# Performance work log

Measured on AMD Instinct MI355X. Metric: run time of the kernel, lower is better.

The kernel has to match this reference:

```python
import jax, jax.numpy as jnp
import numpy as np
from jax import lax

B, T, D, H, L = 16, 256, 128, 128, 4  # batch, seq, input_size, hidden, num_layers
NUM_CLASSES = 10
EPS = 1e-5


def instancenorm(x):
    # x: [B, T, C]; InstanceNorm1d normalizes over the length dim (T) per (B, C),
    # biased variance, eps=1e-5, no affine.
    m = x.mean(axis=1, keepdims=True)
    v = x.var(axis=1, keepdims=True)
    return (x - m) / jnp.sqrt(v + EPS)


def lstm_stack(x, Wih, Whh, bih, bhh):
    # x: [B, T, I]; Wih/Whh: [L, 4H, I_or_H]; bih/bhh: [L, 4H]. Gate order i,f,g,o.
    batch = x.shape[0]
    hid = Whh.shape[-1]
    out = x
    for l in range(Wih.shape[0]):
        wih, whh, b = Wih[l], Whh[l], bih[l] + bhh[l]
        h0 = jnp.zeros((batch, hid), dtype=x.dtype)
        c0 = jnp.zeros((batch, hid), dtype=x.dtype)
        xs = out.swapaxes(0, 1)  # [T, B, I]

        def step(carry, xt):
            h, c = carry
            g = xt @ wih.T + h @ whh.T + b
            i, f, gg, o = jnp.split(g, 4, axis=-1)
            c_new = jax.nn.sigmoid(f) * c + jax.nn.sigmoid(i) * jnp.tanh(gg)
            h_new = jax.nn.sigmoid(o) * jnp.tanh(c_new)
            return (h_new, c_new), h_new

        _, hs = lax.scan(step, (h0, c0), xs)
        out = hs.swapaxes(0, 1)  # [B, T, H]
    return out


def setup_inputs() -> dict:
    key = jax.random.key(0)
    ks = jax.random.split(key, 16)
    s = 1.0 / np.sqrt(H)
    u = lambda k, shape: jax.random.uniform(k, shape, jnp.float32, -s, s)
    return {
        "x": jax.random.normal(ks[0], (B, T, D), jnp.float32),
        "Wih": u(ks[1], (L, 4 * H, D)),   # input_size == hidden_size so shapes stack
        "Whh": u(ks[2], (L, 4 * H, H)),
        "bih": u(ks[3], (L, 4 * H)),
        "bhh": u(ks[4], (L, 4 * H)),
        "proj_h_w": u(ks[5], (H, H)),
        "proj_h_b": u(ks[6], (H,)),
        "proj_x_w": u(ks[7], (H, D)),
        "proj_x_b": u(ks[8], (H,)),
        "attn_w": u(ks[9], (H,)),
        "fc_w": u(ks[10], (NUM_CLASSES, H)),
        "fc_b": u(ks[11], (NUM_CLASSES,)),
    }


def reference(x, Wih, Whh, bih, bhh, proj_h_w, proj_h_b, proj_x_w, proj_x_b, attn_w, fc_w, fc_b):
    batch, seq_len, input_dim = x.shape
    # normalize(): means/stdev are detached; torch std is unbiased (ddof=1)
    means = lax.stop_gradient(x.mean(axis=(0, 1), keepdims=True))
    stdev = lax.stop_gradient(x.std(axis=(0, 1), ddof=1, keepdims=True) + EPS)
    x = (x - means) / stdev
    x = instancenorm(x)

    lstm_out = lstm_stack(x, Wih, Whh, bih, bhh)   # dropout is identity in eval
    lstm_out = instancenorm(lstm_out)

    ph = lstm_out @ proj_h_w.T + proj_h_b           # [B, T, H]
    px = x @ proj_x_w.T + proj_x_b                  # [B, T, H]
    px = instancenorm(px)

    # additive attention over expanded [B, T, D, H] (values identical across D,
    # matching the original broadcast/expand semantics)
    combined = jnp.tanh(
        jnp.broadcast_to((ph + px)[:, :, None, :], (batch, seq_len, input_dim, ph.shape[-1]))
    )
    logits = jnp.einsum("btdh,h->btd", combined, attn_w)       # [B, T, D]
    alpha = jax.nn.softmax(logits.reshape(batch, -1), axis=1)   # softmax over T*D
    attention_map = alpha.reshape(batch, seq_len, input_dim)

    # classify: context = sum over (T, D) of lstm_out_ex * alpha
    context = jnp.einsum("bth,btd->bh", ph, attention_map)      # [B, H]
    out = context @ fc_w.T + fc_b                               # [B, num_classes]
    return out, attention_map
```

## Files before the change

kernel.cpp:

```cpp
#include <hip/hip_runtime.h>
#include <math.h>
#include <cstddef>

#define B_ 16
#define T_ 256
#define D_ 128
#define H_ 128
#define L_ 4
#define G_ 512
#define NC_ 10
#define EPS_ 1e-5f
#define C_ 16
#define NCHUNK_ (T_ / C_)

#define HROW_ 144
#define HOFF(k) ((k) + (((k) >> 5) << 2))

typedef float f4v __attribute__((ext_vector_type(4)));

#define LOAD_W8(w, base)                                                   \
    asm volatile(                                                          \
        "global_load_dwordx4 %0, %8, off\n\t"                             \
        "global_load_dwordx4 %1, %8, off offset:16\n\t"                   \
        "global_load_dwordx4 %2, %8, off offset:32\n\t"                   \
        "global_load_dwordx4 %3, %8, off offset:48\n\t"                   \
        "global_load_dwordx4 %4, %8, off offset:64\n\t"                   \
        "global_load_dwordx4 %5, %8, off offset:80\n\t"                   \
        "global_load_dwordx4 %6, %8, off offset:96\n\t"                   \
        "global_load_dwordx4 %7, %8, off offset:112\n\t"                  \
        "s_waitcnt vmcnt(0)"                                               \
        : "=&v"(w[0]), "=&v"(w[1]), "=&v"(w[2]), "=&v"(w[3]),              \
          "=&v"(w[4]), "=&v"(w[5]), "=&v"(w[6]), "=&v"(w[7])               \
        : "v"(base)                                                        \
        : "memory")

#define DOT32R(dst_, warr_, hvarr_)                                        \
    {                                                                      \
        float d0_ = 0.f, d1_ = 0.f;                                        \
        _Pragma("unroll")                                                  \
        for (int j_ = 0; j_ < 8; j_++) {                                   \
            d0_ = fmaf(warr_[j_].x, hvarr_[j_].x, d0_);                    \
            d1_ = fmaf(warr_[j_].y, hvarr_[j_].y, d1_);                    \
            d0_ = fmaf(warr_[j_].z, hvarr_[j_].z, d0_);                    \
            d1_ = fmaf(warr_[j_].w, hvarr_[j_].w, d1_);                    \
        }                                                                  \
        dst_ = d0_ + d1_;                                                  \
    }

__device__ __forceinline__ float sigmoid_(float x) {
    x = fminf(fmaxf(x, -30.f), 30.f);
    return 1.f / (1.f + __expf(-x));
}
__device__ __forceinline__ float tanh_(float x) {
    float ax = fminf(fabsf(x), 15.f);
    float e = __expf(2.f * ax);
    float t = 1.f - 2.f / (e + 1.f);
    return copysignf(t, x);
}
__device__ __forceinline__ void wait_ge_(int* p, int v) {
    if (__hip_atomic_load(p, __ATOMIC_RELAXED, __HIP_MEMORY_SCOPE_AGENT) < v) {
        do { __builtin_amdgcn_s_sleep(1); }
        while (__hip_atomic_load(p, __ATOMIC_RELAXED, __HIP_MEMORY_SCOPE_AGENT) < v);
    }
    (void)__hip_atomic_load(p, __ATOMIC_ACQUIRE, __HIP_MEMORY_SCOPE_AGENT);
}

__global__ __launch_bounds__(512) void stats_bd(const float* __restrict__ x,
                                                float* __restrict__ sum_bd,
                                                float* __restrict__ sq_bd) {
    int b = blockIdx.x;
    int tid = threadIdx.x;
    int d = tid & 127, r = tid >> 7;
    const float* xb = x + (size_t)b * T_ * D_;
    float s = 0.f, q = 0.f;
    for (int t = r; t < T_; t += 4) {
        float v = xb[t * D_ + d];
        s += v; q += v * v;
    }
    __shared__ float ls[512], lq[512];
    ls[tid] = s; lq[tid] = q;
    __syncthreads();
    if (r == 0) {
        s = ls[d] + ls[d + 128] + ls[d + 256] + ls[d + 384];
        q = lq[d] + lq[d + 128] + lq[d + 256] + lq[d + 384];
        sum_bd[b * 128 + d] = s;
        sq_bd[b * 128 + d] = q;
    }
}

__global__ __launch_bounds__(128) void stats_d(const float* __restrict__ sum_bd,
                                               const float* __restrict__ sq_bd,
                                               float* __restrict__ sdv) {
    int d = threadIdx.x;
    float s = 0.f, q = 0.f;
    for (int b = 0; b < B_; b++) { s += sum_bd[b * 128 + d]; q += sq_bd[b * 128 + d]; }
    float n = (float)(B_ * T_);
    float m = s / n;
    float varu = (q - n * m * m) / (n - 1.f);
    varu = fmaxf(varu, 0.f);
    sdv[d] = sqrtf(varu) + EPS_;
}

__global__ __launch_bounds__(256) void normalize_x(const float* __restrict__ x,
                                                   const float* __restrict__ sum_bd,
                                                   const float* __restrict__ sq_bd,
                                                   const float* __restrict__ sdv,
                                                   float* __restrict__ xn) {
    int idx = blockIdx.x * 256 + threadIdx.x;
    int d = idx & 127;
    int b = idx >> 15;
    int bd = b * 128 + d;
    float mu = sum_bd[bd] * (1.f / T_);
    float varT = sq_bd[bd] * (1.f / T_) - mu * mu;
    float s = sdv[d];
    float inv = rsqrtf(fmaxf(varT, 0.f) + EPS_ * s * s);
    xn[idx] = (x[idx] - mu) * inv;
}

__global__ __launch_bounds__(256) void gemm_bias_k128(const float* __restrict__ A,
                                                      const float* __restrict__ Bw,
                                                      const float* __restrict__ b1,
                                                      const float* __restrict__ b2,
                                                      float* __restrict__ C, int N) {
    __shared__ __align__(16) float As[16][64];
    __shared__ __align__(16) float Bs[16][64];
    int tid = threadIdx.x;
    int m0 = blockIdx.x * 64, n0 = blockIdx.y * 64;
    int lr = tid >> 2;
    int lc = (tid & 3) << 2;
    int tm = (tid >> 4) << 2;
    int tn = (tid & 15) << 2;
    float acc[4][4] = {};
    const float* Arow = A + (size_t)(m0 + lr) * 128 + lc;
    const float* Brow = Bw + (size_t)(n0 + lr) * 128 + lc;
    for (int kb = 0; kb < 128; kb += 16) {
        float4 av = *(const float4*)(Arow + kb);
        float4 bv = *(const float4*)(Brow + kb);
        __syncthreads();
        As[lc + 0][lr] = av.x; As[lc + 1][lr] = av.y; As[lc + 2][lr] = av.z; As[lc + 3][lr] = av.w;
        Bs[lc + 0][lr] = bv.x; Bs[lc + 1][lr] = bv.y; Bs[lc + 2][lr] = bv.z; Bs[lc + 3][lr] = bv.w;
        __syncthreads();
#pragma unroll
        for (int k = 0; k < 16; k++) {
            float4 a4 = *(const float4*)&As[k][tm];
            float4 b4 = *(const float4*)&Bs[k][tn];
            float ar[4] = {a4.x, a4.y, a4.z, a4.w};
            float br[4] = {b4.x, b4.y, b4.z, b4.w};
#pragma unroll
            for (int i = 0; i < 4; i++)
#pragma unroll
                for (int j = 0; j < 4; j++)
                    acc[i][j] = fmaf(ar[i], br[j], acc[i][j]);
        }
    }
#pragma unroll
    for (int i = 0; i < 4; i++) {
        int row = m0 + tm + i;
#pragma unroll
        for (int j = 0; j < 4; j++) {
            int col = n0 + tn + j;
            float bias = b1[col] + (b2 ? b2[col] : 0.f);
            C[(size_t)row * N + col] = acc[i][j] + bias;
        }
    }
}

__global__ __launch_bounds__(256) void gemm_norm_k128(const float* __restrict__ A,
                                                      const float* __restrict__ mu,
                                                      const float* __restrict__ inv,
                                                      const float* __restrict__ Bw,
                                                      const float* __restrict__ b1,
                                                      float* __restrict__ C, int N) {
    __shared__ __align__(16) float As[16][64];
    __shared__ __align__(16) float Bs[16][64];
    int tid = threadIdx.x;
    int m0 = blockIdx.x * 64, n0 = blockIdx.y * 64;
    int lr = tid >> 2;
    int lc = (tid & 3) << 2;
    int tm = (tid >> 4) << 2;
    int tn = (tid & 15) << 2;
    float acc[4][4] = {};
    int bidx = (m0 + lr) >> 8;
    const float* Arow = A + (size_t)(m0 + lr) * 128 + lc;
    const float* Brow = Bw + (size_t)(n0 + lr) * 128 + lc;
    const float* mup = mu + bidx * 128 + lc;
    const float* ivp = inv + bidx * 128 + lc;
    for (int kb = 0; kb < 128; kb += 16) {
        float4 av = *(const float4*)(Arow + kb);
        float4 m4 = *(const float4*)(mup + kb);
        float4 i4 = *(const float4*)(ivp + kb);
        av.x = (av.x - m4.x) * i4.x; av.y = (av.y - m4.y) * i4.y;
        av.z = (av.z - m4.z) * i4.z; av.w = (av.w - m4.w) * i4.w;
        float4 bv = *(const float4*)(Brow + kb);
        __syncthreads();
        As[lc + 0][lr] = av.x; As[lc + 1][lr] = av.y; As[lc + 2][lr] = av.z; As[lc + 3][lr] = av.w;
        Bs[lc + 0][lr] = bv.x; Bs[lc + 1][lr] = bv.y; Bs[lc + 2][lr] = bv.z; Bs[lc + 3][lr] = bv.w;
        __syncthreads();
#pragma unroll
        for (int k = 0; k < 16; k++) {
            float4 a4 = *(const float4*)&As[k][tm];
            float4 b4 = *(const float4*)&Bs[k][tn];
            float ar[4] = {a4.x, a4.y, a4.z, a4.w};
            float br[4] = {b4.x, b4.y, b4.z, b4.w};
#pragma unroll
            for (int i = 0; i < 4; i++)
#pragma unroll
                for (int j = 0; j < 4; j++)
                    acc[i][j] = fmaf(ar[i], br[j], acc[i][j]);
        }
    }
#pragma unroll
    for (int i = 0; i < 4; i++) {
        int row = m0 + tm + i;
#pragma unroll
        for (int j = 0; j < 4; j++) {
            int col = n0 + tn + j;
            C[(size_t)row * N + col] = acc[i][j] + b1[col];
        }
    }
}

__global__ __attribute__((amdgpu_waves_per_eu(2, 2))) __launch_bounds__(512)
void scan_pipe4(const float* __restrict__ g0,
                const float* __restrict__ Wih, const float* __restrict__ Whh,
                const float* __restrict__ bih, const float* __restrict__ bhh,
                float* __restrict__ h_glob,
                float* __restrict__ ring,
                int* __restrict__ flag_h,
                int* __restrict__ flag_g) {
    const int wg = blockIdx.x;
    const int tid = threadIdx.x;
    const int r = tid >> 2, q = tid & 3;

    if (wg < 64) {
        const int l = wg >> 4, b = wg & 15;
        __shared__ __align__(16) float hsh[2][HROW_];
        f4v w0[8], w1[8], w2[8], w3[8];
        const float* wl = Whh + (size_t)l * G_ * 128;
        LOAD_W8(w0, wl + ((size_t)(0 * 128 + r)) * 128 + q * 32);
        LOAD_W8(w1, wl + ((size_t)(1 * 128 + r)) * 128 + q * 32);
        LOAD_W8(w2, wl + ((size_t)(2 * 128 + r)) * 128 + q * 32);
        LOAD_W8(w3, wl + ((size_t)(3 * 128 + r)) * 128 + q * 32);
        float c = 0.f;
        if (tid < HROW_) hsh[0][tid] = 0.f;
        const float* g0p = g0 + (size_t)b * T_ * G_;
        const float* rsl = (l > 0) ? ring + ((size_t)(l - 1) * 16 + b) * (4 * C_ * G_) : ring;
        float* hob = h_glob + ((size_t)l * 16 + b) * T_ * 128;
        int* fg = (l > 0) ? flag_g + (l - 1) * 16 + b : flag_g;
        int* fh = flag_h + l * 16 + b;
        float hreg[C_];
        __syncthreads();

        for (int k = 0; k < NCHUNK_; k++) {
            if (l > 0) {
                if (tid == 0) wait_ge_(fg, k + 1);
                __syncthreads();
            }
#pragma unroll
            for (int half = 0; half < 2; half++) {
                float p0[8], p1[8], p2[8], p3[8];
#pragma unroll
                for (int s8 = 0; s8 < 8; s8++) {
                    int s = half * 8 + s8;
                    if (l == 0) {
                        const float* gp = g0p + (size_t)(k * C_ + s) * G_;
                        p0[s8] = gp[r]; p1[s8] = gp[128 + r];
                        p2[s8] = gp[256 + r]; p3[s8] = gp[384 + r];
                    } else {
                        const float* gp = rsl + ((size_t)(k & 3) * C_ + s) * G_;
                        p0[s8] = __hip_atomic_load(gp + r, __ATOMIC_RELAXED, __HIP_MEMORY_SCOPE_AGENT);
                        p1[s8] = __hip_atomic_load(gp + 128 + r, __ATOMIC_RELAXED, __HIP_MEMORY_SCOPE_AGENT);
                        p2[s8] = __hip_atomic_load(gp + 256 + r, __ATOMIC_RELAXED, __HIP_MEMORY_SCOPE_AGENT);
                        p3[s8] = __hip_atomic_load(gp + 384 + r, __ATOMIC_RELAXED, __HIP_MEMORY_SCOPE_AGENT);
                    }
                }
#pragma unroll
                for (int s8 = 0; s8 < 8; s8++) {
                    int s = half * 8 + s8;
                    int t = k * C_ + s;
                    const f4v* hb4 = (const f4v*)(hsh[t & 1] + q * 36);
                    f4v hv[8];
#pragma unroll
                    for (int j = 0; j < 8; j++) hv[j] = hb4[j];
                    float zi, zf, zg, zo;
                    DOT32R(zi, w0, hv);
                    DOT32R(zf, w1, hv);
                    DOT32R(zg, w2, hv);
                    DOT32R(zo, w3, hv);
                    zi += __shfl_xor(zi, 1); zi += __shfl_xor(zi, 2);
                    zf += __shfl_xor(zf, 1); zf += __shfl_xor(zf, 2);
                    zg += __shfl_xor(zg, 1); zg += __shfl_xor(zg, 2);
                    zo += __shfl_xor(zo, 1); zo += __shfl_xor(zo, 2);
                    zi += p0[s8]; zf += p1[s8]; zg += p2[s8]; zo += p3[s8];
                    float ai = sigmoid_(zi), af = sigmoid_(zf);
                    float ag = tanh_(zg),    ao = sigmoid_(zo);
                    c = fmaf(af, c, ai * ag);
                    float hn = ao * tanh_(c);
                    if (q == 0) hsh[(t + 1) & 1][HOFF(r)] = hn;
                    hreg[s] = hn;
                    __syncthreads();
                }
            }
            if (q == 0) {
#pragma unroll
                for (int s = 0; s < C_; s++)
                    __hip_atomic_store(hob + (size_t)(k * C_ + s) * 128 + r, hreg[s],
                                       __ATOMIC_RELAXED, __HIP_MEMORY_SCOPE_AGENT);
            }
            __syncthreads();
            if (tid == 0) __hip_atomic_store(fh, k + 1, __ATOMIC_RELEASE, __HIP_MEMORY_SCOPE_AGENT);
        }
    } else {
        const int li = (wg - 64) >> 4;
        const int l = li + 1, b = (wg - 64) & 15;
        __shared__ __align__(16) float hch[C_][HROW_];
        f4v w0[8], w1[8], w2[8], w3[8];
        const float* wl = Wih + (size_t)l * G_ * 128;
        LOAD_W8(w0, wl + ((size_t)(0 * 128 + r)) * 128 + q * 32);
        LOAD_W8(w1, wl + ((size_t)(1 * 128 + r)) * 128 + q * 32);
        LOAD_W8(w2, wl + ((size_t)(2 * 128 + r)) * 128 + q * 32);
        LOAD_W8(w3, wl + ((size_t)(3 * 128 + r)) * 128 + q * 32);
        float bs0 = bih[l * G_ + r] + bhh[l * G_ + r];
        float bs1 = bih[l * G_ + 128 + r] + bhh[l * G_ + 128 + r];
        float bs2 = bih[l * G_ + 256 + r] + bhh[l * G_ + 256 + r];
        float bs3 = bih[l * G_ + 384 + r] + bhh[l * G_ + 384 + r];
        const float* hsrc = h_glob + ((size_t)(l - 1) * 16 + b) * T_ * 128;
        float* rout = ring + ((size_t)li * 16 + b) * (4 * C_ * G_);
        int* fhp = flag_h + (l - 1) * 16 + b;
        int* fhme = flag_h + l * 16 + b;
        int* fgo = flag_g + li * 16 + b;

        for (int k = 0; k < NCHUNK_; k++) {
            if (tid == 0) {
                wait_ge_(fhp, k + 1);
                if (k >= 4) wait_ge_(fhme, k - 3);
            }
            __syncthreads();
            {
#pragma unroll
                for (int i = 0; i < 4; i++) {
                    int idx = i * 512 + tid;
                    hch[idx >> 7][HOFF(idx & 127)] =
                        __hip_atomic_load(hsrc + (size_t)k * C_ * 128 + idx,
                                          __ATOMIC_RELAXED, __HIP_MEMORY_SCOPE_AGENT);
                }
            }
            __syncthreads();
#pragma unroll
            for (int s = 0; s < C_; s++) {
                const f4v* hb4 = (const f4v*)(hch[s] + q * 36);
                f4v hv[8];
#pragma unroll
                for (int j = 0; j < 8; j++) hv[j] = hb4[j];
                float z0, z1, z2, z3;
                DOT32R(z0, w0, hv);
                DOT32R(z1, w1, hv);
                DOT32R(z2, w2, hv);
                DOT32R(z3, w3, hv);
                z0 += __shfl_xor(z0, 1); z0 += __shfl_xor(z0, 2);
                z1 += __shfl_xor(z1, 1); z1 += __shfl_xor(z1, 2);
                z2 += __shfl_xor(z2, 1); z2 += __shfl_xor(z2, 2);
                z3 += __shfl_xor(z3, 1); z3 += __shfl_xor(z3, 2);
                if (q == 0) {
                    float* ro = rout + ((size_t)(k & 3) * C_ + s) * G_;
                    __hip_atomic_store(ro + r, z0 + bs0, __ATOMIC_RELAXED, __HIP_MEMORY_SCOPE_AGENT);
                    __hip_atomic_store(ro + 128 + r, z1 + bs1, __ATOMIC_RELAXED, __HIP_MEMORY_SCOPE_AGENT);
                    __hip_atomic_store(ro + 256 + r, z2 + bs2, __ATOMIC_RELAXED, __HIP_MEMORY_SCOPE_AGENT);
                    __hip_atomic_store(ro + 384 + r, z3 + bs3, __ATOMIC_RELAXED, __HIP_MEMORY_SCOPE_AGENT);
                }
            }
            __syncthreads();
            if (tid == 0) __hip_atomic_store(fgo, k + 1, __ATOMIC_RELEASE, __HIP_MEMORY_SCOPE_AGENT);
        }
    }
}

__global__ __launch_bounds__(512) void in_stats(const float* __restrict__ in,
                                                float* __restrict__ mu,
                                                float* __restrict__ inv) {
    int b = blockIdx.x;
    int tid = threadIdx.x;
    int h = tid & 127, r = tid >> 7;
    const float* ib = in + (size_t)b * T_ * H_;
    float s = 0.f, q = 0.f;
    for (int t = r; t < T_; t += 4) { float v = ib[t * H_ + h]; s += v; q += v * v; }
    __shared__ float ls[512], lq[512];
    ls[tid] = s; lq[tid] = q;
    __syncthreads();
    if (r == 0) {
        s = ls[h] + ls[h + 128] + ls[h + 256] + ls[h + 384];
        q = lq[h] + lq[h + 128] + lq[h + 256] + lq[h + 384];
        float m = s * (1.f / T_);
        float v = q * (1.f / T_) - m * m;
        mu[b * 128 + h] = m;
        inv[b * 128 + h] = rsqrtf(fmaxf(v, 0.f) + EPS_);
    }
}

__global__ __launch_bounds__(256) void mega_tail(const float* __restrict__ ph,
                                                 const float* __restrict__ px,
                                                 const float* __restrict__ attn_w,
                                                 const float* __restrict__ fc_w,
                                                 const float* __restrict__ fc_b,
                                                 float* __restrict__ out,
                                                 float* __restrict__ out_att) {
    int b = blockIdx.x;
    int tid = threadIdx.x;
    int h = tid & 127, st = tid >> 7;
    int wv = tid >> 6, ln = tid & 63;
    const float* pxb = px + (size_t)b * T_ * H_;
    const float* phb = ph + (size_t)b * T_ * H_;
    __shared__ float muS[128], invS[128];
    __shared__ float ls[256], lq[256];
    __shared__ float lsc[256], tmp[256], wsh[256];

    {
        float s = 0.f, q = 0.f;
        for (int t = st; t < T_; t += 2) { float v = pxb[t * 128 + h]; s += v; q += v * v; }
        ls[tid] = s; lq[tid] = q;
        __syncthreads();
        if (st == 0) {
            s = ls[h] + ls[h + 128]; q = lq[h] + lq[h + 128];
            float m = s * (1.f / T_);
            float v = q * (1.f / T_) - m * m;
            muS[h] = m;
            invS[h] = rsqrtf(fmaxf(v, 0.f) + EPS_);
        }
        __syncthreads();
    }
    for (int t4 = 0; t4 < T_; t4 += 4) {
        int t = t4 + wv;
        float v0 = phb[t * 128 + ln] + (pxb[t * 128 + ln] - muS[ln]) * invS[ln];
        float v1 = phb[t * 128 + 64 + ln] + (pxb[t * 128 + 64 + ln] - muS[64 + ln]) * invS[64 + ln];
        float sv = tanh_(v0) * attn_w[ln] + tanh_(v1) * attn_w[64 + ln];
#pragma unroll
        for (int off = 32; off > 0; off >>= 1) sv += __shfl_down(sv, off);
        if (ln == 0) lsc[t] = sv;
    }
    __syncthreads();
    {
        float v = lsc[tid];
        tmp[tid] = v; __syncthreads();
        for (int off = 128; off > 0; off >>= 1) { if (tid < off) tmp[tid] = fmaxf(tmp[tid], tmp[tid + off]); __syncthreads(); }
        float mx = tmp[0]; __syncthreads();
        float e = __expf(v - mx);
        tmp[tid] = e; __syncthreads();
        for (int off = 128; off > 0; off >>= 1) { if (tid < off) tmp[tid] += tmp[tid + off]; __syncthreads(); }
        wsh[tid] = e / tmp[0];
        __syncthreads();
    }
    {
        float* ob = out_att + (size_t)b * T_ * D_;
        const float invD = 1.f / (float)D_;
        for (int i = tid; i < T_ * D_; i += 256) ob[i] = wsh[i >> 7] * invD;
    }
    {
        float acc = 0.f;
        for (int t = st; t < T_; t += 2) acc = fmaf(phb[t * 128 + h], wsh[t], acc);
        ls[tid] = acc;
        __syncthreads();
        if (tid < 128) ls[tid] = ls[tid] + ls[tid + 128];
        __syncthreads();
        if (tid < NC_) {
            float s = fc_b[tid];
            const float* fw = fc_w + tid * 128;
            for (int k = 0; k < 128; k++) s = fmaf(ls[k], fw[k], s);
            out[b * NC_ + tid] = s;
        }
    }
}

extern "C" void kernel_launch(void* const* d_in, const int* in_sizes, int n_in,
                              void* d_out, int out_size, void* d_ws, size_t ws_size,
                              hipStream_t stream) {
    const float* x        = (const float*)d_in[0];
    const float* Wih      = (const float*)d_in[1];
    const float* Whh      = (const float*)d_in[2];
    const float* bih      = (const float*)d_in[3];
    const float* bhh      = (const float*)d_in[4];
    const float* proj_h_w = (const float*)d_in[5];
    const float* proj_h_b = (const float*)d_in[6];
    const float* proj_x_w = (const float*)d_in[7];
    const float* proj_x_b = (const float*)d_in[8];
    const float* attn_w   = (const float*)d_in[9];
    const float* fc_w     = (const float*)d_in[10];
    const float* fc_b     = (const float*)d_in[11];
    float* out = (float*)d_out;

    float* ws = (float*)d_ws;
    const size_t NTD = (size_t)B_ * T_ * D_;
    float* xnorm  = ws;
    float* h_glob = xnorm + NTD;
    float* g0     = h_glob + 4 * NTD;
    float* ring   = g0 + 4 * NTD;
    float* smalls = ring + (size_t)3 * 16 * 4 * C_ * G_;
    float* sum_bd = smalls;
    float* sq_bd  = sum_bd + 2048;
    float* sdv    = sq_bd + 2048;
    float* mu_ln  = sdv + 128;
    float* inv_ln = mu_ln + 2048;
    int*   flags  = (int*)(inv_ln + 2048);
    int*   flag_h = flags;
    int*   flag_g = flags + 64;
    float* ph    = h_glob;
    float* px    = h_glob + NTD;
    const float* h3 = h_glob + 3 * NTD;

    hipMemsetAsync((void*)flags, 0, 128 * sizeof(int), stream);

    stats_bd<<<16, 512, 0, stream>>>(x, sum_bd, sq_bd);
    stats_d<<<1, 128, 0, stream>>>(sum_bd, sq_bd, sdv);
    normalize_x<<<2048, 256, 0, stream>>>(x, sum_bd, sq_bd, sdv, xnorm);

    dim3 g1(64, 8);
    gemm_bias_k128<<<g1, 256, 0, stream>>>(xnorm, Wih, bih, bhh, g0, G_);
    scan_pipe4<<<112, 512, 0, stream>>>(g0, Wih, Whh, bih, bhh,
                                        h_glob, ring, flag_h, flag_g);

    in_stats<<<16, 512, 0, stream>>>(h3, mu_ln, inv_ln);
    dim3 g2(64, 2);
    gemm_norm_k128<<<g2, 256, 0, stream>>>(h3, mu_ln, inv_ln, proj_h_w, proj_h_b, ph, H_);
    gemm_bias_k128<<<g2, 256, 0, stream>>>(xnorm, proj_x_w, proj_x_b, nullptr, px, H_);

    mega_tail<<<16, 256, 0, stream>>>(ph, px, attn_w, fc_w, fc_b, out, out + B_ * NC_);
}
```

Measured before the change: 562.3 us.

## Fold input normalization into GEMM and overlap projection and stats with LSTM scan

```diff
diff --git a/kernel.cpp b/kernel.cpp
--- a/kernel.cpp
+++ b/kernel.cpp
@@ -88,80 +88,22 @@
     }
 }
 
-__global__ __launch_bounds__(128) void stats_d(const float* __restrict__ sum_bd,
-                                               const float* __restrict__ sq_bd,
-                                               float* __restrict__ sdv) {
+__global__ __launch_bounds__(128) void stats_norm(const float* __restrict__ sum_bd,
+                                                  const float* __restrict__ sq_bd,
+                                                  float* __restrict__ mu_bd,
+                                                  float* __restrict__ invn) {
     int d = threadIdx.x;
     float s = 0.f, q = 0.f;
     for (int b = 0; b < B_; b++) { s += sum_bd[b * 128 + d]; q += sq_bd[b * 128 + d]; }
     float n = (float)(B_ * T_);
     float m = s / n;
     float varu = (q - n * m * m) / (n - 1.f);
-    varu = fmaxf(varu, 0.f);
-    sdv[d] = sqrtf(varu) + EPS_;
-}
-
-__global__ __launch_bounds__(256) void normalize_x(const float* __restrict__ x,
-                                                   const float* __restrict__ sum_bd,
-                                                   const float* __restrict__ sq_bd,
-                                                   const float* __restrict__ sdv,
-                                                   float* __restrict__ xn) {
-    int idx = blockIdx.x * 256 + threadIdx.x;
-    int d = idx & 127;
-    int b = idx >> 15;
-    int bd = b * 128 + d;
-    float mu = sum_bd[bd] * (1.f / T_);
-    float varT = sq_bd[bd] * (1.f / T_) - mu * mu;
-    float s = sdv[d];
-    float inv = rsqrtf(fmaxf(varT, 0.f) + EPS_ * s * s);
-    xn[idx] = (x[idx] - mu) * inv;
-}
-
-__global__ __launch_bounds__(256) void gemm_bias_k128(const float* __restrict__ A,
-                                                      const float* __restrict__ Bw,
-                                                      const float* __restrict__ b1,
-                                                      const float* __restrict__ b2,
-                                                      float* __restrict__ C, int N) {
-    __shared__ __align__(16) float As[16][64];
-    __shared__ __align__(16) float Bs[16][64];
-    int tid = threadIdx.x;
-    int m0 = blockIdx.x * 64, n0 = blockIdx.y * 64;
-    int lr = tid >> 2;
-    int lc = (tid & 3) << 2;
-    int tm = (tid >> 4) << 2;
-    int tn = (tid & 15) << 2;
-    float acc[4][4] = {};
-    const float* Arow = A + (size_t)(m0 + lr) * 128 + lc;
-    const float* Brow = Bw + (size_t)(n0 + lr) * 128 + lc;
-    for (int kb = 0; kb < 128; kb += 16) {
-        float4 av = *(const float4*)(Arow + kb);
-        float4 bv = *(const float4*)(Brow + kb);
-        __syncthreads();
-        As[lc + 0][lr] = av.x; As[lc + 1][lr] = av.y; As[lc + 2][lr] = av.z; As[lc + 3][lr] = av.w;
-        Bs[lc + 0][lr] = bv.x; Bs[lc + 1][lr] = bv.y; Bs[lc + 2][lr] = bv.z; Bs[lc + 3][lr] = bv.w;
-        __syncthreads();
-#pragma unroll
-        for (int k = 0; k < 16; k++) {
-            float4 a4 = *(const float4*)&As[k][tm];
-            float4 b4 = *(const float4*)&Bs[k][tn];
-            float ar[4] = {a4.x, a4.y, a4.z, a4.w};
-            float br[4] = {b4.x, b4.y, b4.z, b4.w};
-#pragma unroll
-            for (int i = 0; i < 4; i++)
-#pragma unroll
-                for (int j = 0; j < 4; j++)
-                    acc[i][j] = fmaf(ar[i], br[j], acc[i][j]);
-        }
-    }
-#pragma unroll
-    for (int i = 0; i < 4; i++) {
-        int row = m0 + tm + i;
-#pragma unroll
-        for (int j = 0; j < 4; j++) {
-            int col = n0 + tn + j;
-            float bias = b1[col] + (b2 ? b2[col] : 0.f);
-            C[(size_t)row * N + col] = acc[i][j] + bias;
-        }
+    float sd = sqrtf(fmaxf(varu, 0.f)) + EPS_;
+    for (int b = 0; b < B_; b++) {
+        float mu = sum_bd[b * 128 + d] * (1.f / T_);
+        float varT = sq_bd[b * 128 + d] * (1.f / T_) - mu * mu;
+        mu_bd[b * 128 + d] = mu;
+        invn[b * 128 + d] = rsqrtf(fmaxf(varT, 0.f) + EPS_ * sd * sd);
     }
 }
 
@@ -170,6 +112,7 @@
                                                       const float* __restrict__ inv,
                                                       const float* __restrict__ Bw,
                                                       const float* __restrict__ b1,
+                                                      const float* __restrict__ b2,
                                                       float* __restrict__ C, int N) {
     __shared__ __align__(16) float As[16][64];
     __shared__ __align__(16) float Bs[16][64];
@@ -215,26 +158,33 @@
 #pragma unroll
         for (int j = 0; j < 4; j++) {
             int col = n0 + tn + j;
-            C[(size_t)row * N + col] = acc[i][j] + b1[col];
+            float bias = b1[col] + (b2 ? b2[col] : 0.f);
+            C[(size_t)row * N + col] = acc[i][j] + bias;
         }
     }
 }
 
 __global__ __attribute__((amdgpu_waves_per_eu(2, 2))) __launch_bounds__(512)
-void scan_pipe4(const float* __restrict__ g0,
+void scan_pipe5(const float* __restrict__ g0,
+                const float* __restrict__ x,
                 const float* __restrict__ Wih, const float* __restrict__ Whh,
                 const float* __restrict__ bih, const float* __restrict__ bhh,
+                const float* __restrict__ proj_x_w, const float* __restrict__ proj_x_b,
+                const float* __restrict__ mu_bd, const float* __restrict__ invn,
                 float* __restrict__ h_glob,
                 float* __restrict__ ring,
+                float* __restrict__ px,
+                float* __restrict__ mu_px, float* __restrict__ inv_px,
+                float* __restrict__ mu_ln, float* __restrict__ inv_ln,
                 int* __restrict__ flag_h,
                 int* __restrict__ flag_g) {
     const int wg = blockIdx.x;
     const int tid = threadIdx.x;
-    const int r = tid >> 2, q = tid & 3;
+    __shared__ __align__(16) float shbuf[16 * HROW_];
 
     if (wg < 64) {
+        const int r = tid >> 2, q = tid & 3;
         const int l = wg >> 4, b = wg & 15;
-        __shared__ __align__(16) float hsh[2][HROW_];
         f4v w0[8], w1[8], w2[8], w3[8];
         const float* wl = Whh + (size_t)l * G_ * 128;
         LOAD_W8(w0, wl + ((size_t)(0 * 128 + r)) * 128 + q * 32);
@@ -242,7 +192,7 @@
         LOAD_W8(w2, wl + ((size_t)(2 * 128 + r)) * 128 + q * 32);
         LOAD_W8(w3, wl + ((size_t)(3 * 128 + r)) * 128 + q * 32);
         float c = 0.f;
-        if (tid < HROW_) hsh[0][tid] = 0.f;
+        if (tid < HROW_) shbuf[tid] = 0.f;
         const float* g0p = g0 + (size_t)b * T_ * G_;
         const float* rsl = (l > 0) ? ring + ((size_t)(l - 1) * 16 + b) * (4 * C_ * G_) : ring;
         float* hob = h_glob + ((size_t)l * 16 + b) * T_ * 128;
@@ -278,7 +228,7 @@
                 for (int s8 = 0; s8 < 8; s8++) {
                     int s = half * 8 + s8;
                     int t = k * C_ + s;
-                    const f4v* hb4 = (const f4v*)(hsh[t & 1] + q * 36);
+                    const f4v* hb4 = (const f4v*)(shbuf + (t & 1) * HROW_ + q * 36);
                     f4v hv[8];
 #pragma unroll
                     for (int j = 0; j < 8; j++) hv[j] = hb4[j];
@@ -296,7 +246,7 @@
                     float ag = tanh_(zg),    ao = sigmoid_(zo);
                     c = fmaf(af, c, ai * ag);
                     float hn = ao * tanh_(c);
-                    if (q == 0) hsh[(t + 1) & 1][HOFF(r)] = hn;
+                    if (q == 0) shbuf[((t + 1) & 1) * HROW_ + HOFF(r)] = hn;
                     hreg[s] = hn;
                     __syncthreads();
                 }
@@ -310,10 +260,10 @@
             __syncthreads();
             if (tid == 0) __hip_atomic_store(fh, k + 1, __ATOMIC_RELEASE, __HIP_MEMORY_SCOPE_AGENT);
         }
-    } else {
+    } else if (wg < 112) {
+        const int r = tid >> 2, q = tid & 3;
         const int li = (wg - 64) >> 4;
         const int l = li + 1, b = (wg - 64) & 15;
-        __shared__ __align__(16) float hch[C_][HROW_];
         f4v w0[8], w1[8], w2[8], w3[8];
         const float* wl = Wih + (size_t)l * G_ * 128;
         LOAD_W8(w0, wl + ((size_t)(0 * 128 + r)) * 128 + q * 32);
@@ -336,19 +286,17 @@
                 if (k >= 4) wait_ge_(fhme, k - 3);
             }
             __syncthreads();
-            {
-#pragma unroll
-                for (int i = 0; i < 4; i++) {
-                    int idx = i * 512 + tid;
-                    hch[idx >> 7][HOFF(idx & 127)] =
-                        __hip_atomic_load(hsrc + (size_t)k * C_ * 128 + idx,
-                                          __ATOMIC_RELAXED, __HIP_MEMORY_SCOPE_AGENT);
-                }
+#pragma unroll
+            for (int i = 0; i < 4; i++) {
+                int idx = i * 512 + tid;
+                shbuf[(idx >> 7) * HROW_ + HOFF(idx & 127)] =
+                    __hip_atomic_load(hsrc + (size_t)k * C_ * 128 + idx,
+                                      __ATOMIC_RELAXED, __HIP_MEMORY_SCOPE_AGENT);
             }
             __syncthreads();
 #pragma unroll
             for (int s = 0; s < C_; s++) {
-                const f4v* hb4 = (const f4v*)(hch[s] + q * 36);
+                const f4v* hb4 = (const f4v*)(shbuf + s * HROW_ + q * 36);
                 f4v hv[8];
 #pragma unroll
                 for (int j = 0; j < 8; j++) hv[j] = hb4[j];
@@ -372,83 +320,142 @@
             __syncthreads();
             if (tid == 0) __hip_atomic_store(fgo, k + 1, __ATOMIC_RELEASE, __HIP_MEMORY_SCOPE_AGENT);
         }
-    }
-}
-
-__global__ __launch_bounds__(512) void in_stats(const float* __restrict__ in,
-                                                float* __restrict__ mu,
-                                                float* __restrict__ inv) {
-    int b = blockIdx.x;
-    int tid = threadIdx.x;
-    int h = tid & 127, r = tid >> 7;
-    const float* ib = in + (size_t)b * T_ * H_;
-    float s = 0.f, q = 0.f;
-    for (int t = r; t < T_; t += 4) { float v = ib[t * H_ + h]; s += v; q += v * v; }
-    __shared__ float ls[512], lq[512];
-    ls[tid] = s; lq[tid] = q;
+    } else if (wg < 128) {
+        const int b = wg - 112;
+        const int h = tid & 127, tq = tid >> 7;
+        f4v w0[8], w1[8], w2[8], w3[8];
+        LOAD_W8(w0, proj_x_w + (size_t)h * 128 + 0);
+        LOAD_W8(w1, proj_x_w + (size_t)h * 128 + 32);
+        LOAD_W8(w2, proj_x_w + (size_t)h * 128 + 64);
+        LOAD_W8(w3, proj_x_w + (size_t)h * 128 + 96);
+        float bsx = proj_x_b[h];
+        float muk = mu_bd[b * 128 + h], ivk = invn[b * 128 + h];
+        const float* xb = x + (size_t)b * T_ * 128;
+        float* pxb = px + (size_t)b * T_ * 128;
+        float sacc = 0.f, qacc = 0.f;
+
+        for (int blk = 0; blk < 16; blk++) {
+            int t0 = blk * 16;
+            __syncthreads();
+#pragma unroll
+            for (int j = 0; j < 4; j++) {
+                int tt = tq * 4 + j;
+                float v = xb[(size_t)(t0 + tt) * 128 + h];
+                shbuf[tt * HROW_ + HOFF(h)] = (v - muk) * ivk;
+            }
+            __syncthreads();
+#pragma unroll
+            for (int j = 0; j < 4; j++) {
+                int tt = tq * 4 + j;
+                const float* row = shbuf + tt * HROW_;
+                f4v hv[8];
+                float p0, p1, p2, p3;
+                const f4v* r4 = (const f4v*)(row + 0 * 36);
+#pragma unroll
+                for (int u = 0; u < 8; u++) hv[u] = r4[u];
+                DOT32R(p0, w0, hv);
+                r4 = (const f4v*)(row + 1 * 36);
+#pragma unroll
+                for (int u = 0; u < 8; u++) hv[u] = r4[u];
+                DOT32R(p1, w1, hv);
+                r4 = (const f4v*)(row + 2 * 36);
+#pragma unroll
+                for (int u = 0; u < 8; u++) hv[u] = r4[u];
+                DOT32R(p2, w2, hv);
+                r4 = (const f4v*)(row + 3 * 36);
+#pragma unroll
+                for (int u = 0; u < 8; u++) hv[u] = r4[u];
+                DOT32R(p3, w3, hv);
+                float val = (p0 + p1) + (p2 + p3) + bsx;
+                pxb[(size_t)(t0 + tt) * 128 + h] = val;
+                sacc += val; qacc += val * val;
+            }
+        }
+        __syncthreads();
+        shbuf[tq * 128 + h] = sacc;
+        shbuf[512 + tq * 128 + h] = qacc;
+        __syncthreads();
+        if (tq == 0) {
+            float s = shbuf[h] + shbuf[128 + h] + shbuf[256 + h] + shbuf[384 + h];
+            float qq = shbuf[512 + h] + shbuf[640 + h] + shbuf[768 + h] + shbuf[896 + h];
+            float m = s * (1.f / T_);
+            float v = qq * (1.f / T_) - m * m;
+            mu_px[b * 128 + h] = m;
+            inv_px[b * 128 + h] = rsqrtf(fmaxf(v, 0.f) + EPS_);
+        }
+    } else {
+        const int b = wg - 128;
+        const int h = tid & 127, st = tid >> 7;
+        const float* hsrc = h_glob + ((size_t)3 * 16 + b) * T_ * 128;
+        int* f3 = flag_h + 3 * 16 + b;
+        float s = 0.f, q = 0.f;
+        for (int k = 0; k < NCHUNK_; k++) {
+            if (tid == 0) wait_ge_(f3, k + 1);
+            __syncthreads();
+#pragma unroll
+            for (int j = 0; j < 4; j++) {
+                int tt = st * 4 + j;
+                float v = __hip_atomic_load(hsrc + (size_t)(k * C_ + tt) * 128 + h,
+                                            __ATOMIC_RELAXED, __HIP_MEMORY_SCOPE_AGENT);
+                s += v; q += v * v;
+            }
+        }
+        shbuf[st * 128 + h] = s;
+        shbuf[512 + st * 128 + h] = q;
+        __syncthreads();
+        if (st == 0) {
+            float ss = shbuf[h] + shbuf[128 + h] + shbuf[256 + h] + shbuf[384 + h];
+            float qq = shbuf[512 + h] + shbuf[640 + h] + shbuf[768 + h] + shbuf[896 + h];
+            float m = ss * (1.f / T_);
+            float v = qq * (1.f / T_) - m * m;
+            mu_ln[b * 128 + h] = m;
+            inv_ln[b * 128 + h] = rsqrtf(fmaxf(v, 0.f) + EPS_);
+        }
+    }
+}
+
+__global__ __launch_bounds__(128) void score_kernel(const float* __restrict__ ph,
+                                                    const float* __restrict__ px,
+                                                    const float* __restrict__ mu_px,
+                                                    const float* __restrict__ inv_px,
+                                                    const float* __restrict__ attn_w,
+                                                    float* __restrict__ lsc) {
+    int bt = blockIdx.x;
+    int b = bt >> 8;
+    int h = threadIdx.x;
+    size_t o = (size_t)bt * 128 + h;
+    float v = ph[o] + (px[o] - mu_px[b * 128 + h]) * inv_px[b * 128 + h];
+    float sv = tanh_(v) * attn_w[h];
+    __shared__ float red[128];
+    red[h] = sv;
     __syncthreads();
-    if (r == 0) {
-        s = ls[h] + ls[h + 128] + ls[h + 256] + ls[h + 384];
-        q = lq[h] + lq[h + 128] + lq[h + 256] + lq[h + 384];
-        float m = s * (1.f / T_);
-        float v = q * (1.f / T_) - m * m;
-        mu[b * 128 + h] = m;
-        inv[b * 128 + h] = rsqrtf(fmaxf(v, 0.f) + EPS_);
-    }
-}
-
-__global__ __launch_bounds__(256) void mega_tail(const float* __restrict__ ph,
-                                                 const float* __restrict__ px,
-                                                 const float* __restrict__ attn_w,
-                                                 const float* __restrict__ fc_w,
-                                                 const float* __restrict__ fc_b,
-                                                 float* __restrict__ out,
-                                                 float* __restrict__ out_att) {
+    for (int off = 64; off > 0; off >>= 1) {
+        if (h < off) red[h] += red[h + off];
+        __syncthreads();
+    }
+    if (h == 0) lsc[bt] = red[0];
+}
+
+__global__ __launch_bounds__(256) void tail3(const float* __restrict__ lsc,
+                                             const float* __restrict__ ph,
+                                             const float* __restrict__ fc_w,
+                                             const float* __restrict__ fc_b,
+                                             float* __restrict__ out,
+                                             float* __restrict__ out_att) {
     int b = blockIdx.x;
     int tid = threadIdx.x;
     int h = tid & 127, st = tid >> 7;
-    int wv = tid >> 6, ln = tid & 63;
-    const float* pxb = px + (size_t)b * T_ * H_;
     const float* phb = ph + (size_t)b * T_ * H_;
-    __shared__ float muS[128], invS[128];
-    __shared__ float ls[256], lq[256];
-    __shared__ float lsc[256], tmp[256], wsh[256];
-
-    {
-        float s = 0.f, q = 0.f;
-        for (int t = st; t < T_; t += 2) { float v = pxb[t * 128 + h]; s += v; q += v * v; }
-        ls[tid] = s; lq[tid] = q;
-        __syncthreads();
-        if (st == 0) {
-            s = ls[h] + ls[h + 128]; q = lq[h] + lq[h + 128];
-            float m = s * (1.f / T_);
-            float v = q * (1.f / T_) - m * m;
-            muS[h] = m;
-            invS[h] = rsqrtf(fmaxf(v, 0.f) + EPS_);
-        }
-        __syncthreads();
-    }
-    for (int t4 = 0; t4 < T_; t4 += 4) {
-        int t = t4 + wv;
-        float v0 = phb[t * 128 + ln] + (pxb[t * 128 + ln] - muS[ln]) * invS[ln];
-        float v1 = phb[t * 128 + 64 + ln] + (pxb[t * 128 + 64 + ln] - muS[64 + ln]) * invS[64 + ln];
-        float sv = tanh_(v0) * attn_w[ln] + tanh_(v1) * attn_w[64 + ln];
-#pragma unroll
-        for (int off = 32; off > 0; off >>= 1) sv += __shfl_down(sv, off);
-        if (ln == 0) lsc[t] = sv;
-    }
+    __shared__ float tmp[256], wsh[256], ls[256];
+    float v = lsc[b * 256 + tid];
+    tmp[tid] = v; __syncthreads();
+    for (int off = 128; off > 0; off >>= 1) { if (tid < off) tmp[tid] = fmaxf(tmp[tid], tmp[tid + off]); __syncthreads(); }
+    float mx = tmp[0]; __syncthreads();
+    float e = __expf(v - mx);
+    tmp[tid] = e; __syncthreads();
+    for (int off = 128; off > 0; off >>= 1) { if (tid < off) tmp[tid] += tmp[tid + off]; __syncthreads(); }
+    wsh[tid] = e / tmp[0];
     __syncthreads();
-    {
-        float v = lsc[tid];
-        tmp[tid] = v; __syncthreads();
-        for (int off = 128; off > 0; off >>= 1) { if (tid < off) tmp[tid] = fmaxf(tmp[tid], tmp[tid + off]); __syncthreads(); }
-        float mx = tmp[0]; __syncthreads();
-        float e = __expf(v - mx);
-        tmp[tid] = e; __syncthreads();
-        for (int off = 128; off > 0; off >>= 1) { if (tid < off) tmp[tid] += tmp[tid + off]; __syncthreads(); }
-        wsh[tid] = e / tmp[0];
-        __syncthreads();
-    }
     {
         float* ob = out_att + (size_t)b * T_ * D_;
         const float invD = 1.f / (float)D_;
@@ -489,38 +496,42 @@
 
     float* ws = (float*)d_ws;
     const size_t NTD = (size_t)B_ * T_ * D_;
-    float* xnorm  = ws;
-    float* h_glob = xnorm + NTD;
+    float* h_glob = ws;
     float* g0     = h_glob + 4 * NTD;
     float* ring   = g0 + 4 * NTD;
-    float* smalls = ring + (size_t)3 * 16 * 4 * C_ * G_;
+    float* px     = ring + 3 * NTD;
+    float* smalls = px + NTD;
     float* sum_bd = smalls;
     float* sq_bd  = sum_bd + 2048;
-    float* sdv    = sq_bd + 2048;
-    float* mu_ln  = sdv + 128;
+    float* mu_bd  = sq_bd + 2048;
+    float* invn   = mu_bd + 2048;
+    float* mu_ln  = invn + 2048;
     float* inv_ln = mu_ln + 2048;
-    int*   flags  = (int*)(inv_ln + 2048);
+    float* mu_px  = inv_ln + 2048;
+    float* inv_px = mu_px + 2048;
+    float* lsc    = inv_px + 2048;
+    int*   flags  = (int*)(lsc + 4096);
     int*   flag_h = flags;
     int*   flag_g = flags + 64;
-    float* ph    = h_glob;
-    float* px    = h_glob + NTD;
+    float* ph = h_glob;
     const float* h3 = h_glob + 3 * NTD;
 
     hipMemsetAsync((void*)flags, 0, 128 * sizeof(int), stream);
 
     stats_bd<<<16, 512, 0, stream>>>(x, sum_bd, sq_bd);
-    stats_d<<<1, 128, 0, stream>>>(sum_bd, sq_bd, sdv);
-    normalize_x<<<2048, 256, 0, stream>>>(x, sum_bd, sq_bd, sdv, xnorm);
-
+    stats_norm<<<1, 128, 0, stream>>>(sum_bd, sq_bd, mu_bd, invn);
     dim3 g1(64, 8);
-    gemm_bias_k128<<<g1, 256, 0, stream>>>(xnorm, Wih, bih, bhh, g0, G_);
-    scan_pipe4<<<112, 512, 0, stream>>>(g0, Wih, Whh, bih, bhh,
-                                        h_glob, ring, flag_h, flag_g);
-
-    in_stats<<<16, 512, 0, stream>>>(h3, mu_ln, inv_ln);
+    gemm_norm_k128<<<g1, 256, 0, stream>>>(x, mu_bd, invn, Wih, bih, bhh, g0, G_);
+
+    scan_pipe5<<<144, 512, 0, stream>>>(g0, x, Wih, Whh, bih, bhh,
+                                        proj_x_w, proj_x_b, mu_bd, invn,
+                                        h_glob, ring, px, mu_px, inv_px,
+                                        mu_ln, inv_ln, flag_h, flag_g);
+
     dim3 g2(64, 2);
-    gemm_norm_k128<<<g2, 256, 0, stream>>>(h3, mu_ln, inv_ln, proj_h_w, proj_h_b, ph, H_);
-    gemm_bias_k128<<<g2, 256, 0, stream>>>(xnorm, proj_x_w, proj_x_b, nullptr, px, H_);
-
-    mega_tail<<<16, 256, 0, stream>>>(ph, px, attn_w, fc_w, fc_b, out, out + B_ * NC_);
-}
+    gemm_norm_k128<<<g2, 256, 0, stream>>>(h3, mu_ln, inv_ln, proj_h_w, proj_h_b,
+                                           nullptr, ph, H_);
+
+    score_kernel<<<4096, 128, 0, stream>>>(ph, px, mu_px, inv_px, attn_w, lsc);
+    tail3<<<16, 256, 0, stream>>>(lsc, ph, fc_w, fc_b, out, out + B_ * NC_);
+}
```

Result: faster. 497.8 us (-11.5%).
